# Performance work log

Hardware: AMD Instinct MI355X
Metric: run time of the kernel (lower is better)

## Reference

```python
import jax, jax.numpy as jnp
import numpy as np

RANKS = [16, 16, 16, 16]
ALPHAS = [32.0, 32.0, 32.0, 32.0]
IN_DIM, OUT_DIM = 4096, 4096
BSZ, SEQ = 4, 2048


def _col_scale(dtype):
    # per-column scale alpha_i / rank_i for each adapter's rank block
    s = np.concatenate([np.full(r, a / r, dtype=np.float32) for r, a in zip(RANKS, ALPHAS)])
    return jnp.asarray(s, dtype=dtype)


def setup_inputs() -> dict:
    key = jax.random.key(0)
    k1, k2, k3, k4 = jax.random.split(key, 4)
    total_rank = sum(RANKS)
    x = jax.random.normal(k1, (BSZ, SEQ, IN_DIM), dtype=jnp.float32)
    weight = jax.random.normal(k2, (OUT_DIM, IN_DIM), dtype=jnp.float32) * (1.0 / np.sqrt(IN_DIM))
    lora_a_weight = jax.random.normal(k3, (total_rank, IN_DIM), dtype=jnp.float32) * (1.0 / np.sqrt(IN_DIM))
    lora_b_weight = jax.random.normal(k4, (OUT_DIM, total_rank), dtype=jnp.float32) * 0.02
    return {"x": x, "weight": weight, "lora_a_weight": lora_a_weight, "lora_b_weight": lora_b_weight}


def reference(x, weight, lora_a_weight, lora_b_weight):
    # base: F.linear(x, W) -> x @ W^T        [B,S,out_dim]
    out = jnp.einsum('bsi,oi->bso', x, weight)
    # lora_a: x @ A^T                         [B,S,sum_rank] (dropout p=0 -> no-op)
    lora_a_out = jnp.einsum('bsi,ri->bsr', x, lora_a_weight)
    # The per-adapter masked loop sum_i (alpha_i/r_i) * (lora_a_out * mask_i) @ B^T
    # is mathematically a single GEMM with per-column scaling of lora_a_out.
    scaled = lora_a_out * _col_scale(lora_a_out.dtype)
    lora_out_total = jnp.einsum('bsr,or->bso', scaled, lora_b_weight)
    return out + lora_out_total
```

## Files before the change

kernel.cpp:

```cpp
#include <hip/hip_runtime.h>

typedef __bf16 bf16_t;
typedef __attribute__((ext_vector_type(8))) __bf16 bf16x8;
typedef __attribute__((ext_vector_type(4))) float f32x4;

#define M_DIM 8192
#define N_DIM 4096
#define K_DIM 4096
#define R_DIM 64

__global__ __launch_bounds__(256) void cvt_x(const float* __restrict__ in,
                                             bf16_t* __restrict__ out) {
    size_t i = ((size_t)blockIdx.x * 256 + threadIdx.x) * 8;
    float4 a = *(const float4*)(in + i);
    float4 b = *(const float4*)(in + i + 4);
    bf16x8 v;
    v[0] = (bf16_t)a.x; v[1] = (bf16_t)a.y; v[2] = (bf16_t)a.z; v[3] = (bf16_t)a.w;
    v[4] = (bf16_t)b.x; v[5] = (bf16_t)b.y; v[6] = (bf16_t)b.z; v[7] = (bf16_t)b.w;
    *(bf16x8*)(out + i) = v;
}

__global__ __launch_bounds__(256) void build_weff(const float* __restrict__ W,
                                                  const float* __restrict__ A,
                                                  const float* __restrict__ Bl,
                                                  bf16_t* __restrict__ out) {
    const int i  = blockIdx.x * 256 + threadIdx.x;
    const int o0 = blockIdx.y * 16;

    float acc[16];
#pragma unroll
    for (int j = 0; j < 16; j++) acc[j] = W[(size_t)(o0 + j) * K_DIM + i];

    for (int rh = 0; rh < R_DIM; rh += 16) {
        float av[16];
#pragma unroll
        for (int r = 0; r < 16; r++) av[r] = 2.0f * A[(size_t)(rh + r) * K_DIM + i];
#pragma unroll
        for (int j = 0; j < 16; j++) {
#pragma unroll
            for (int r = 0; r < 16; r++)
                acc[j] += Bl[(o0 + j) * R_DIM + rh + r] * av[r];
        }
    }
#pragma unroll
    for (int j = 0; j < 16; j++) out[(size_t)(o0 + j) * K_DIM + i] = (bf16_t)acc[j];
}

#define BM 128
#define BN 128
#define BK 64

#define GLDS(gp, lp) __builtin_amdgcn_global_load_lds(                       \
    (__attribute__((address_space(1))) void*)(gp),                           \
    (__attribute__((address_space(3))) void*)(lp), 16, 0, 0)

__global__ __launch_bounds__(256) void gemm_bf16(const bf16_t* __restrict__ Ax,
                                                 const bf16_t* __restrict__ Bw,
                                                 float* __restrict__ C) {
    __shared__ __attribute__((aligned(16))) bf16_t Ash[BM * BK];
    __shared__ __attribute__((aligned(16))) bf16_t Bsh[BN * BK];

    const int tid  = threadIdx.x;
    const int wave = tid >> 6;
    const int lane = tid & 63;
    const int m16  = lane & 15;
    const int quad = lane >> 4;
    const int wm   = wave >> 1;
    const int wn   = wave & 1;
    const int m0 = blockIdx.y * BM;
    const int n0 = blockIdx.x * BN;

    f32x4 acc[4][4] = {};

    const int srow   = lane >> 3;
    const int schunk = lane & 7;

    for (int k0 = 0; k0 < K_DIM; k0 += BK) {
        __syncthreads();
#pragma unroll
        for (int i = 0; i < 4; i++) {
            const int rb = (i * 4 + wave) * 8;
            const int r  = rb + srow;
            const int ca = schunk ^ (r & 7);
            GLDS(Ax + (size_t)(m0 + r) * K_DIM + k0 + ca * 8, Ash + rb * BK);
            GLDS(Bw + (size_t)(n0 + r) * K_DIM + k0 + ca * 8, Bsh + rb * BK);
        }
        __syncthreads();
#pragma unroll
        for (int ks = 0; ks < 2; ks++) {
            bf16x8 afr[4], bfr[4];
#pragma unroll
            for (int t = 0; t < 4; t++) {
                const int mr = wm * 64 + t * 16 + m16;
                const int nr = wn * 64 + t * 16 + m16;
                const int ck = ks * 4 + quad;
                afr[t] = *(const bf16x8*)(Ash + mr * BK + ((ck ^ (mr & 7)) << 3));
                bfr[t] = *(const bf16x8*)(Bsh + nr * BK + ((ck ^ (nr & 7)) << 3));
            }
#pragma unroll
            for (int tm = 0; tm < 4; tm++)
#pragma unroll
                for (int tn = 0; tn < 4; tn++)
                    acc[tm][tn] = __builtin_amdgcn_mfma_f32_16x16x32_bf16(
                        afr[tm], bfr[tn], acc[tm][tn], 0, 0, 0);
        }
    }

#pragma unroll
    for (int tm = 0; tm < 4; tm++) {
#pragma unroll
        for (int i = 0; i < 4; i++) {
            const int gm = m0 + wm * 64 + tm * 16 + quad * 4 + i;
            float* crow = C + (size_t)gm * N_DIM + n0 + wn * 64 + m16;
#pragma unroll
            for (int tn = 0; tn < 4; tn++)
                crow[tn * 16] = acc[tm][tn][i];
        }
    }
}

extern "C" void kernel_launch(void* const* d_in, const int* in_sizes, int n_in,
                              void* d_out, int out_size, void* d_ws, size_t ws_size,
                              hipStream_t stream) {
    const float* x  = (const float*)d_in[0];
    const float* W  = (const float*)d_in[1];
    const float* La = (const float*)d_in[2];
    const float* Lb = (const float*)d_in[3];
    float* out = (float*)d_out;

    bf16_t* xb = (bf16_t*)d_ws;
    bf16_t* wf = (bf16_t*)((char*)d_ws + (size_t)M_DIM * K_DIM * sizeof(bf16_t));

    cvt_x<<<(M_DIM * K_DIM) / (256 * 8), 256, 0, stream>>>(x, xb);
    build_weff<<<dim3(K_DIM / 256, N_DIM / 16), 256, 0, stream>>>(W, La, Lb, wf);
    gemm_bf16<<<dim3(N_DIM / BN, M_DIM / BM), 256, 0, stream>>>(xb, wf, out);
}
```

Before: 609.7 us.

## Warp-specialize GEMM with producer wave and double-buffered LDS tiles

Replaces the barrier-synchronised single-buffer GEMM with a 320-thread block. A dedicated producer wave streams A and B tiles into two LDS buffers with global_load_lds, while four consumer waves run the MFMAs. The two sides coordinate through ready/done counters in LDS using atomics and s_sleep spin loops rather than __syncthreads, so the next tile's loads can overlap compute on the current one. In exchange, LDS use doubles, which may lower occupancy, and correctness now depends on the counters. The done counter is incremented by every lane of each consumer wave, which looks like it could let the producer overwrite a buffer before all consumer waves have finished reading it.

```diff
diff --git a/kernel.cpp b/kernel.cpp
--- a/kernel.cpp
+++ b/kernel.cpp
@@ -49,53 +49,84 @@
 #define BM 128
 #define BN 128
 #define BK 64
+#define KT (K_DIM / BK)
 
 #define GLDS(gp, lp) __builtin_amdgcn_global_load_lds(                       \
     (__attribute__((address_space(1))) void*)(gp),                           \
     (__attribute__((address_space(3))) void*)(lp), 16, 0, 0)
 
-__global__ __launch_bounds__(256) void gemm_bf16(const bf16_t* __restrict__ Ax,
-                                                 const bf16_t* __restrict__ Bw,
-                                                 float* __restrict__ C) {
-    __shared__ __attribute__((aligned(16))) bf16_t Ash[BM * BK];
-    __shared__ __attribute__((aligned(16))) bf16_t Bsh[BN * BK];
+__global__ __launch_bounds__(320) void gemm_pc(const bf16_t* __restrict__ Ax,
+                                               const bf16_t* __restrict__ Bw,
+                                               float* __restrict__ C) {
+    __shared__ __attribute__((aligned(16))) bf16_t Ash[2][BM * BK];
+    __shared__ __attribute__((aligned(16))) bf16_t Bsh[2][BN * BK];
+    __shared__ int ready[2];
+    __shared__ int done[2];
 
     const int tid  = threadIdx.x;
     const int wave = tid >> 6;
     const int lane = tid & 63;
+    const int m0 = blockIdx.y * BM;
+    const int n0 = blockIdx.x * BN;
+
+    if (tid == 0) { ready[0] = ready[1] = 0; done[0] = done[1] = 0; }
+    __syncthreads();
+
+    if (wave == 4) {
+        const int srow   = lane >> 3;
+        const int schunk = lane & 7;
+        for (int t = 0; t < KT; t++) {
+            const int b = t & 1, n = t >> 1;
+            if (t >= 2) {
+                while (__hip_atomic_load(&done[b], __ATOMIC_ACQUIRE,
+                                         __HIP_MEMORY_SCOPE_WORKGROUP) < 4 * n)
+                    __builtin_amdgcn_s_sleep(1);
+            }
+            const int k0 = t * BK;
+#pragma unroll
+            for (int i = 0; i < 16; i++) {
+                const int rb = i * 8;
+                const int r  = rb + srow;
+                const int ca = schunk ^ (r & 7);
+                GLDS(Ax + (size_t)(m0 + r) * K_DIM + k0 + ca * 8, &Ash[b][rb * BK]);
+            }
+#pragma unroll
+            for (int i = 0; i < 16; i++) {
+                const int rb = i * 8;
+                const int r  = rb + srow;
+                const int ca = schunk ^ (r & 7);
+                GLDS(Bw + (size_t)(n0 + r) * K_DIM + k0 + ca * 8, &Bsh[b][rb * BK]);
+            }
+            __builtin_amdgcn_s_waitcnt(0x0f70);
+            if (lane == 0)
+                __hip_atomic_store(&ready[b], n + 1, __ATOMIC_RELEASE,
+                                   __HIP_MEMORY_SCOPE_WORKGROUP);
+        }
+        return;
+    }
+
     const int m16  = lane & 15;
     const int quad = lane >> 4;
     const int wm   = wave >> 1;
     const int wn   = wave & 1;
-    const int m0 = blockIdx.y * BM;
-    const int n0 = blockIdx.x * BN;
 
     f32x4 acc[4][4] = {};
 
-    const int srow   = lane >> 3;
-    const int schunk = lane & 7;
-
-    for (int k0 = 0; k0 < K_DIM; k0 += BK) {
-        __syncthreads();
-#pragma unroll
-        for (int i = 0; i < 4; i++) {
-            const int rb = (i * 4 + wave) * 8;
-            const int r  = rb + srow;
-            const int ca = schunk ^ (r & 7);
-            GLDS(Ax + (size_t)(m0 + r) * K_DIM + k0 + ca * 8, Ash + rb * BK);
-            GLDS(Bw + (size_t)(n0 + r) * K_DIM + k0 + ca * 8, Bsh + rb * BK);
-        }
-        __syncthreads();
+    for (int t = 0; t < KT; t++) {
+        const int b = t & 1, n = t >> 1;
+        while (__hip_atomic_load(&ready[b], __ATOMIC_ACQUIRE,
+                                 __HIP_MEMORY_SCOPE_WORKGROUP) < n + 1)
+            __builtin_amdgcn_s_sleep(1);
 #pragma unroll
         for (int ks = 0; ks < 2; ks++) {
             bf16x8 afr[4], bfr[4];
 #pragma unroll
-            for (int t = 0; t < 4; t++) {
-                const int mr = wm * 64 + t * 16 + m16;
-                const int nr = wn * 64 + t * 16 + m16;
+            for (int tt = 0; tt < 4; tt++) {
+                const int mr = wm * 64 + tt * 16 + m16;
+                const int nr = wn * 64 + tt * 16 + m16;
                 const int ck = ks * 4 + quad;
-                afr[t] = *(const bf16x8*)(Ash + mr * BK + ((ck ^ (mr & 7)) << 3));
-                bfr[t] = *(const bf16x8*)(Bsh + nr * BK + ((ck ^ (nr & 7)) << 3));
+                afr[tt] = *(const bf16x8*)(&Ash[b][mr * BK + ((ck ^ (mr & 7)) << 3)]);
+                bfr[tt] = *(const bf16x8*)(&Bsh[b][nr * BK + ((ck ^ (nr & 7)) << 3)]);
             }
 #pragma unroll
             for (int tm = 0; tm < 4; tm++)
@@ -104,6 +135,8 @@
                     acc[tm][tn] = __builtin_amdgcn_mfma_f32_16x16x32_bf16(
                         afr[tm], bfr[tn], acc[tm][tn], 0, 0, 0);
         }
+        __hip_atomic_fetch_add(&done[b], 1, __ATOMIC_RELEASE,
+                               __HIP_MEMORY_SCOPE_WORKGROUP);
     }
 
 #pragma unroll
@@ -133,5 +166,5 @@
 
     cvt_x<<<(M_DIM * K_DIM) / (256 * 8), 256, 0, stream>>>(x, xb);
     build_weff<<<dim3(K_DIM / 256, N_DIM / 16), 256, 0, stream>>>(W, La, Lb, wf);
-    gemm_bf16<<<dim3(N_DIM / BN, M_DIM / BM), 256, 0, stream>>>(xb, wf, out);
+    gemm_pc<<<dim3(N_DIM / BN, M_DIM / BM), 320, 0, stream>>>(xb, wf, out);
 }
```

Measured after the change: 762.6 us. 25.1% more time.
